# Performance work log

Hardware: AMD Instinct MI355X
Metric: run time of the kernel (lower is better)

Reference implementation:

```python
import jax, jax.numpy as jnp
import numpy as np

P = 0.5
SCALE_TRUE = 10.0
SCALE_WRONG = -10.0
B, C = 2048, 50257


def setup_inputs() -> dict:
    key = jax.random.key(0)
    k1, k2 = jax.random.split(key)
    output = jax.random.normal(k1, (B, C), dtype=jnp.float32)
    labels = jax.random.randint(k2, (B,), 0, C, dtype=jnp.int64)
    return {"output": output, "labels": labels}


def reference(output, labels):
    b, c = output.shape
    rows = jnp.arange(b)

    # tempOut: positive logits scaled by scale_wrong, else 0
    temp_out = jnp.where(output > 0, output * SCALE_WRONG, jnp.zeros_like(output))

    # tempLabels: filled with scale_wrong; target entry per row set to
    # max(|mean(row)|, |row[label]|) * scale_true
    gathered = output[rows, labels]                     # [B]
    row_val = jnp.maximum(jnp.abs(jnp.mean(output, axis=1)), jnp.abs(gathered)) * SCALE_TRUE
    temp_labels = jnp.full_like(output, SCALE_WRONG).at[rows, labels].set(row_val)

    # L1 loss (mean reduction over all elements)
    l1 = jnp.mean(jnp.abs(temp_out - temp_labels))

    # Cross-entropy (mean over batch)
    log_probs = jax.nn.log_softmax(output, axis=1)      # [B, C]
    ce = -jnp.mean(log_probs[rows, labels])

    return P * l1 + (1.0 - P) * ce
```

## Files before the change

### kernel.cpp

```cpp
#include <hip/hip_runtime.h>
#include <stdint.h>

#define BATCH 2048
#define NCLS  50257
#define LOG2E 1.44269504088896340736f
#define LN2   0.69314718055994530942f

typedef float v4f __attribute__((ext_vector_type(4)));

__device__ __forceinline__ float l1_base(float v) {
    return fabsf(1.f - fmaxf(v, 0.f));
}

__global__ __launch_bounds__(256) void custom_loss_kernel(
    const float* __restrict__ x,
    const int*   __restrict__ labels,
    float*       __restrict__ result)
{
    const int row = blockIdx.x;
    const int tid = threadIdx.x;
    const float* rp = x + (size_t)row * NCLS;

    float s0=0.f, s1=0.f, s2=0.f, s3=0.f;
    float a0=0.f, a1=0.f, a2=0.f, a3=0.f;
    float e0=0.f, e1=0.f, e2=0.f, e3=0.f;

    const int peel_full = (int)(((16u - ((uintptr_t)rp & 15u)) & 15u) >> 2);
    const int peel = peel_full > NCLS ? NCLS : peel_full;
    if (tid < peel) {
        float v = rp[tid];
        s0 += v; a0 += l1_base(v); e0 += exp2f(v * LOG2E);
    }

    const v4f* rp4 = (const v4f*)(rp + peel);
    const int n4 = (NCLS - peel) >> 2;
    int i = tid;
    for (; i + 768 < n4; i += 1024) {
        v4f a = __builtin_nontemporal_load(&rp4[i]);
        v4f b = __builtin_nontemporal_load(&rp4[i + 256]);
        v4f c = __builtin_nontemporal_load(&rp4[i + 512]);
        v4f d = __builtin_nontemporal_load(&rp4[i + 768]);

        s0 += (a.x + a.y) + (a.z + a.w);
        s1 += (b.x + b.y) + (b.z + b.w);
        s2 += (c.x + c.y) + (c.z + c.w);
        s3 += (d.x + d.y) + (d.z + d.w);

        a0 += (l1_base(a.x) + l1_base(a.y)) + (l1_base(a.z) + l1_base(a.w));
        a1 += (l1_base(b.x) + l1_base(b.y)) + (l1_base(b.z) + l1_base(b.w));
        a2 += (l1_base(c.x) + l1_base(c.y)) + (l1_base(c.z) + l1_base(c.w));
        a3 += (l1_base(d.x) + l1_base(d.y)) + (l1_base(d.z) + l1_base(d.w));

        e0 += (exp2f(a.x * LOG2E) + exp2f(a.y * LOG2E))
            + (exp2f(a.z * LOG2E) + exp2f(a.w * LOG2E));
        e1 += (exp2f(b.x * LOG2E) + exp2f(b.y * LOG2E))
            + (exp2f(b.z * LOG2E) + exp2f(b.w * LOG2E));
        e2 += (exp2f(c.x * LOG2E) + exp2f(c.y * LOG2E))
            + (exp2f(c.z * LOG2E) + exp2f(c.w * LOG2E));
        e3 += (exp2f(d.x * LOG2E) + exp2f(d.y * LOG2E))
            + (exp2f(d.z * LOG2E) + exp2f(d.w * LOG2E));
    }
    for (; i < n4; i += 256) {
        v4f a = __builtin_nontemporal_load(&rp4[i]);
        s0 += (a.x + a.y) + (a.z + a.w);
        a0 += (l1_base(a.x) + l1_base(a.y)) + (l1_base(a.z) + l1_base(a.w));
        e0 += (exp2f(a.x * LOG2E) + exp2f(a.y * LOG2E))
            + (exp2f(a.z * LOG2E) + exp2f(a.w * LOG2E));
    }

    const int tail = peel + (n4 << 2);
    for (int j = tail + tid; j < NCLS; j += 256) {
        float v = rp[j];
        s0 += v; a0 += l1_base(v); e0 += exp2f(v * LOG2E);
    }

    float S = (s0 + s1) + (s2 + s3);
    float L = (a0 + a1) + (a2 + a3);
    float E = (e0 + e1) + (e2 + e3);

    #pragma unroll
    for (int off = 32; off > 0; off >>= 1) {
        S += __shfl_down(S, off);
        L += __shfl_down(L, off);
        E += __shfl_down(E, off);
    }

    __shared__ float red[3][4];
    const int lane = tid & 63, wave = tid >> 6;
    if (lane == 0) { red[0][wave] = S; red[1][wave] = L; red[2][wave] = E; }
    __syncthreads();

    if (tid == 0) {
        float Sa = (red[0][0] + red[0][1]) + (red[0][2] + red[0][3]);
        float La = (red[1][0] + red[1][1]) + (red[1][2] + red[1][3]);
        float Ea = (red[2][0] + red[2][1]) + (red[2][2] + red[2][3]);

        const int   label = labels[row];
        const float g     = rp[label];

        const float mean    = Sa * (1.f / (float)NCLS);
        const float row_val = fmaxf(fabsf(mean), fabsf(g)) * 10.f;
        const float tout_g  = (g > 0.f) ? -10.f * g : 0.f;
        const float l1_row  = 10.f * La - 10.f * l1_base(g) + fabsf(tout_g - row_val);

        const float ce_row  = __log2f(Ea) * LN2 - g;

        const float inv_bc = 1.f / ((float)BATCH * (float)NCLS);
        const float inv_b  = 1.f / (float)BATCH;
        const float contrib = 0.5f * l1_row * inv_bc + 0.5f * ce_row * inv_b;

        atomicAdd(result, contrib);
    }
}

extern "C" void kernel_launch(void* const* d_in, const int* in_sizes, int n_in,
                              void* d_out, int out_size, void* d_ws, size_t ws_size,
                              hipStream_t stream) {
    const float* x      = (const float*)d_in[0];
    const int*   labels = (const int*)d_in[1];
    float*       out    = (float*)d_out;

    (void)hipMemsetAsync(out, 0, sizeof(float), stream);

    custom_loss_kernel<<<BATCH, 256, 0, stream>>>(x, labels, out);
}
```

Baseline: 516.6 us.

## Process four rows per 1024-thread block with two-way unrolled loads

```diff
diff --git a/kernel.cpp b/kernel.cpp
--- a/kernel.cpp
+++ b/kernel.cpp
@@ -3,6 +3,9 @@
 
 #define BATCH 2048
 #define NCLS  50257
+#define RPB   4
+#define TPB   1024
+#define NWAVE (TPB/64)
 #define LOG2E 1.44269504088896340736f
 #define LN2   0.69314718055994530942f
 
@@ -12,104 +15,101 @@
     return fabsf(1.f - fmaxf(v, 0.f));
 }
 
-__global__ __launch_bounds__(256) void custom_loss_kernel(
+__global__ __launch_bounds__(TPB, 8) void custom_loss_kernel(
     const float* __restrict__ x,
     const int*   __restrict__ labels,
     float*       __restrict__ result)
 {
-    const int row = blockIdx.x;
-    const int tid = threadIdx.x;
-    const float* rp = x + (size_t)row * NCLS;
+    const int tid  = threadIdx.x;
+    const int row0 = blockIdx.x * RPB;
 
-    float s0=0.f, s1=0.f, s2=0.f, s3=0.f;
-    float a0=0.f, a1=0.f, a2=0.f, a3=0.f;
-    float e0=0.f, e1=0.f, e2=0.f, e3=0.f;
+    __shared__ float red[RPB][3][NWAVE];
 
-    const int peel_full = (int)(((16u - ((uintptr_t)rp & 15u)) & 15u) >> 2);
-    const int peel = peel_full > NCLS ? NCLS : peel_full;
-    if (tid < peel) {
-        float v = rp[tid];
-        s0 += v; a0 += l1_base(v); e0 += exp2f(v * LOG2E);
-    }
+    for (int r = 0; r < RPB; ++r) {
+        const int row = row0 + r;
+        const float* rp = x + (size_t)row * NCLS;
 
-    const v4f* rp4 = (const v4f*)(rp + peel);
-    const int n4 = (NCLS - peel) >> 2;
-    int i = tid;
-    for (; i + 768 < n4; i += 1024) {
-        v4f a = __builtin_nontemporal_load(&rp4[i]);
-        v4f b = __builtin_nontemporal_load(&rp4[i + 256]);
-        v4f c = __builtin_nontemporal_load(&rp4[i + 512]);
-        v4f d = __builtin_nontemporal_load(&rp4[i + 768]);
+        float s0=0.f, s1=0.f;
+        float a0=0.f, a1=0.f;
+        float e0=0.f, e1=0.f;
 
-        s0 += (a.x + a.y) + (a.z + a.w);
-        s1 += (b.x + b.y) + (b.z + b.w);
-        s2 += (c.x + c.y) + (c.z + c.w);
-        s3 += (d.x + d.y) + (d.z + d.w);
+        const int peel_full = (int)(((16u - ((uintptr_t)rp & 15u)) & 15u) >> 2);
+        const int peel = peel_full > NCLS ? NCLS : peel_full;
+        if (tid < peel) {
+            float v = rp[tid];
+            s0 += v; a0 += l1_base(v); e0 += exp2f(v * LOG2E);
+        }
 
-        a0 += (l1_base(a.x) + l1_base(a.y)) + (l1_base(a.z) + l1_base(a.w));
-        a1 += (l1_base(b.x) + l1_base(b.y)) + (l1_base(b.z) + l1_base(b.w));
-        a2 += (l1_base(c.x) + l1_base(c.y)) + (l1_base(c.z) + l1_base(c.w));
-        a3 += (l1_base(d.x) + l1_base(d.y)) + (l1_base(d.z) + l1_base(d.w));
+        const v4f* rp4 = (const v4f*)(rp + peel);
+        const int n4 = (NCLS - peel) >> 2;
+        int i = tid;
+        for (; i + TPB < n4; i += 2 * TPB) {
+            v4f a = __builtin_nontemporal_load(&rp4[i]);
+            v4f b = __builtin_nontemporal_load(&rp4[i + TPB]);
 
-        e0 += (exp2f(a.x * LOG2E) + exp2f(a.y * LOG2E))
-            + (exp2f(a.z * LOG2E) + exp2f(a.w * LOG2E));
-        e1 += (exp2f(b.x * LOG2E) + exp2f(b.y * LOG2E))
-            + (exp2f(b.z * LOG2E) + exp2f(b.w * LOG2E));
-        e2 += (exp2f(c.x * LOG2E) + exp2f(c.y * LOG2E))
-            + (exp2f(c.z * LOG2E) + exp2f(c.w * LOG2E));
-        e3 += (exp2f(d.x * LOG2E) + exp2f(d.y * LOG2E))
-            + (exp2f(d.z * LOG2E) + exp2f(d.w * LOG2E));
-    }
-    for (; i < n4; i += 256) {
-        v4f a = __builtin_nontemporal_load(&rp4[i]);
-        s0 += (a.x + a.y) + (a.z + a.w);
-        a0 += (l1_base(a.x) + l1_base(a.y)) + (l1_base(a.z) + l1_base(a.w));
-        e0 += (exp2f(a.x * LOG2E) + exp2f(a.y * LOG2E))
-            + (exp2f(a.z * LOG2E) + exp2f(a.w * LOG2E));
-    }
+            s0 += (a.x + a.y) + (a.z + a.w);
+            s1 += (b.x + b.y) + (b.z + b.w);
 
-    const int tail = peel + (n4 << 2);
-    for (int j = tail + tid; j < NCLS; j += 256) {
-        float v = rp[j];
-        s0 += v; a0 += l1_base(v); e0 += exp2f(v * LOG2E);
-    }
+            a0 += (l1_base(a.x) + l1_base(a.y)) + (l1_base(a.z) + l1_base(a.w));
+            a1 += (l1_base(b.x) + l1_base(b.y)) + (l1_base(b.z) + l1_base(b.w));
 
-    float S = (s0 + s1) + (s2 + s3);
-    float L = (a0 + a1) + (a2 + a3);
-    float E = (e0 + e1) + (e2 + e3);
+            e0 += (exp2f(a.x * LOG2E) + exp2f(a.y * LOG2E))
+                + (exp2f(a.z * LOG2E) + exp2f(a.w * LOG2E));
+            e1 += (exp2f(b.x * LOG2E) + exp2f(b.y * LOG2E))
+                + (exp2f(b.z * LOG2E) + exp2f(b.w * LOG2E));
+        }
+        for (; i < n4; i += TPB) {
+            v4f a = __builtin_nontemporal_load(&rp4[i]);
+            s0 += (a.x + a.y) + (a.z + a.w);
+            a0 += (l1_base(a.x) + l1_base(a.y)) + (l1_base(a.z) + l1_base(a.w));
+            e0 += (exp2f(a.x * LOG2E) + exp2f(a.y * LOG2E))
+                + (exp2f(a.z * LOG2E) + exp2f(a.w * LOG2E));
+        }
 
-    #pragma unroll
-    for (int off = 32; off > 0; off >>= 1) {
-        S += __shfl_down(S, off);
-        L += __shfl_down(L, off);
-        E += __shfl_down(E, off);
-    }
+        const int tail = peel + (n4 << 2);
+        for (int j = tail + tid; j < NCLS; j += TPB) {
+            float v = rp[j];
+            s0 += v; a0 += l1_base(v); e0 += exp2f(v * LOG2E);
+        }
 
-    __shared__ float red[3][4];
-    const int lane = tid & 63, wave = tid >> 6;
-    if (lane == 0) { red[0][wave] = S; red[1][wave] = L; red[2][wave] = E; }
-    __syncthreads();
+        float S = s0 + s1;
+        float L = a0 + a1;
+        float E = e0 + e1;
 
-    if (tid == 0) {
-        float Sa = (red[0][0] + red[0][1]) + (red[0][2] + red[0][3]);
-        float La = (red[1][0] + red[1][1]) + (red[1][2] + red[1][3]);
-        float Ea = (red[2][0] + red[2][1]) + (red[2][2] + red[2][3]);
+        #pragma unroll
+        for (int off = 32; off > 0; off >>= 1) {
+            S += __shfl_down(S, off);
+            L += __shfl_down(L, off);
+            E += __shfl_down(E, off);
+        }
 
-        const int   label = labels[row];
-        const float g     = rp[label];
+        const int lane = tid & 63, wave = tid >> 6;
+        if (lane == 0) { red[r][0][wave] = S; red[r][1][wave] = L; red[r][2][wave] = E; }
+        __syncthreads();
 
-        const float mean    = Sa * (1.f / (float)NCLS);
-        const float row_val = fmaxf(fabsf(mean), fabsf(g)) * 10.f;
-        const float tout_g  = (g > 0.f) ? -10.f * g : 0.f;
-        const float l1_row  = 10.f * La - 10.f * l1_base(g) + fabsf(tout_g - row_val);
+        if (tid == 0) {
+            float Sa = 0.f, La = 0.f, Ea = 0.f;
+            #pragma unroll
+            for (int w = 0; w < NWAVE; ++w) {
+                Sa += red[r][0][w]; La += red[r][1][w]; Ea += red[r][2][w];
+            }
 
-        const float ce_row  = __log2f(Ea) * LN2 - g;
+            const int   label = labels[row];
+            const float g     = rp[label];
 
-        const float inv_bc = 1.f / ((float)BATCH * (float)NCLS);
-        const float inv_b  = 1.f / (float)BATCH;
-        const float contrib = 0.5f * l1_row * inv_bc + 0.5f * ce_row * inv_b;
+            const float mean    = Sa * (1.f / (float)NCLS);
+            const float row_val = fmaxf(fabsf(mean), fabsf(g)) * 10.f;
+            const float tout_g  = (g > 0.f) ? -10.f * g : 0.f;
+            const float l1_row  = 10.f * La - 10.f * l1_base(g) + fabsf(tout_g - row_val);
 
-        atomicAdd(result, contrib);
+            const float ce_row  = __log2f(Ea) * LN2 - g;
+
+            const float inv_bc = 1.f / ((float)BATCH * (float)NCLS);
+            const float inv_b  = 1.f / (float)BATCH;
+            const float contrib = 0.5f * l1_row * inv_bc + 0.5f * ce_row * inv_b;
+
+            atomicAdd(result, contrib);
+        }
     }
 }
 
@@ -122,5 +122,5 @@
 
     (void)hipMemsetAsync(out, 0, sizeof(float), stream);
 
-    custom_loss_kernel<<<BATCH, 256, 0, stream>>>(x, labels, out);
+    custom_loss_kernel<<<BATCH / RPB, TPB, 0, stream>>>(x, labels, out);
 }
```

Result: faster. 505.8 us (-2.1%).
